# Optimization experiments

Measured on AMD Instinct MI355X. Metric: run time of the kernel, lower is better.

Reference implementation:

```python
import jax, jax.numpy as jnp
import numpy as np

B, S_Q, S_KV, DIM, H = 2, 2048, 2048, 1024, 16
HD = DIM // H
SCALE = HD ** -0.5
EPS = 1e-8


def apply_rope(x, freqs):
    # x: (b, s, h, hd); freqs: (b, s, hd) = [cos | sin] halves of size hd//2
    xr = x.reshape(x.shape[:-1] + (HD // 2, 2))
    x_r, x_i = xr[..., 0], xr[..., 1]
    cos, sin = jnp.split(freqs, 2, axis=-1)          # each (b, s, hd//2)
    cos = cos[:, :, None, :]
    sin = sin[:, :, None, :]
    o_r = x_r * cos - x_i * sin
    o_i = x_r * sin + x_i * cos
    return jnp.stack([o_r, o_i], axis=-1).reshape(x.shape)


def setup_inputs() -> dict:
    key = jax.random.key(0)
    ks = jax.random.split(key, 9)
    q_x = jax.random.normal(ks[0], (B, S_Q, DIM), jnp.float32)
    kv_x = jax.random.normal(ks[1], (B, S_KV, DIM), jnp.float32)
    q_freqs_cis = jax.random.normal(ks[2], (B, S_Q, HD), jnp.float32)
    k_freqs_cis = jax.random.normal(ks[3], (B, S_KV, HD), jnp.float32)
    mask = jnp.zeros((B, 1, S_Q, S_KV), jnp.float32)
    attn_prior = jax.random.uniform(ks[4], (B, S_Q, S_KV), jnp.float32)
    Wq = jax.random.normal(ks[5], (DIM, DIM), jnp.float32) * 0.02
    Wkv = jax.random.normal(ks[6], (2 * DIM, DIM), jnp.float32) * 0.02
    Wproj = jax.random.normal(ks[7], (DIM, DIM), jnp.float32) * 0.02
    bproj = jax.random.normal(ks[8], (DIM,), jnp.float32) * 0.02
    return {"q_x": q_x, "kv_x": kv_x, "q_freqs_cis": q_freqs_cis,
            "k_freqs_cis": k_freqs_cis, "mask": mask, "attn_prior": attn_prior,
            "Wq": Wq, "Wkv": Wkv, "Wproj": Wproj, "bproj": bproj}


def reference(q_x, kv_x, q_freqs_cis, k_freqs_cis, mask, attn_prior,
              Wq, Wkv, Wproj, bproj):
    b, sq, _ = q_x.shape
    skv = kv_x.shape[1]
    q = (q_x @ Wq.T).reshape(b, sq, H, HD)
    kv = (kv_x @ Wkv.T).reshape(b, skv, 2, H, HD)
    k, v = kv[:, :, 0], kv[:, :, 1]
    q = apply_rope(q, q_freqs_cis)
    k = apply_rope(k, k_freqs_cis)
    # scores: (b, h, q, k)
    attn = jnp.einsum("bqhd,bkhd->bhqk", q * SCALE, k)
    attn = attn + mask
    attn = jax.nn.softmax(attn, axis=-1)
    # log-space fusion with multiplicative prior, then renormalize
    prior = attn_prior[:, None, :, :]
    attn = jnp.exp(jnp.log(jnp.clip(attn, EPS)) + jnp.log(jnp.clip(prior, EPS)))
    attn = attn / jnp.sum(attn, axis=-1, keepdims=True)
    x = jnp.einsum("bhqk,bkhd->bqhd", attn, v).reshape(b, sq, DIM)
    x = x @ Wproj.T + bproj
    return (x, attn)
```

## Files before the change

### kernel.cpp

```cpp
#include <hip/hip_runtime.h>
#include <hip/hip_bf16.h>

typedef __bf16 bf16;
typedef __bf16 bf16x4 __attribute__((ext_vector_type(4)));
typedef __bf16 bf16x8 __attribute__((ext_vector_type(8)));
typedef float floatx4 __attribute__((ext_vector_type(4)));
typedef float float4v __attribute__((ext_vector_type(4)));

#define MFMA16(a, b, c) __builtin_amdgcn_mfma_f32_16x16x32_bf16(a, b, c, 0, 0, 0)

constexpr int B_ = 2, S_ = 2048, DIM_ = 1024, H_ = 16, HD_ = 64;
constexpr float SCALE_ = 0.125f;
constexpr float EPS_ = 1e-8f;

__device__ __forceinline__ void gload_lds16(const void* g, void* l) {
    __builtin_amdgcn_global_load_lds(
        (const __attribute__((address_space(1))) void*)g,
        (__attribute__((address_space(3))) void*)l, 16, 0, 0);
}

__global__ __launch_bounds__(256) void prep_kernel(const float* __restrict__ q_x,
                                                   const float* __restrict__ kv_x,
                                                   const float* __restrict__ Wq,
                                                   const float* __restrict__ Wkv,
                                                   const float* __restrict__ Wproj,
                                                   const float* __restrict__ mask,
                                                   const float* __restrict__ prior,
                                                   bf16* __restrict__ qx_b,
                                                   bf16* __restrict__ kvx_b,
                                                   bf16* __restrict__ wq_b,
                                                   bf16* __restrict__ wkv_b,
                                                   bf16* __restrict__ wpj_b,
                                                   float* __restrict__ lp) {
    const int blk = blockIdx.x, t = threadIdx.x;
    auto cvt = [&](const float* in, bf16* out, int base) {
        int i = base * 256 + t;
        float4v v = __builtin_nontemporal_load((const float4v*)in + i);
        bf16x4 o;
#pragma unroll
        for (int j = 0; j < 4; ++j) o[j] = (bf16)v[j];
        ((bf16x4*)out)[i] = o;
    };
    if (blk < 4096)        cvt(q_x,   qx_b,  blk);
    else if (blk < 8192)   cvt(kv_x,  kvx_b, blk - 4096);
    else if (blk < 9216)   cvt(Wq,    wq_b,  blk - 8192);
    else if (blk < 11264)  cvt(Wkv,   wkv_b, blk - 9216);
    else if (blk < 12288)  cvt(Wproj, wpj_b, blk - 11264);
    else {
        int i = (blk - 12288) * 256 + t;
        float4v m = __builtin_nontemporal_load((const float4v*)mask + i);
        float4v p = __builtin_nontemporal_load((const float4v*)prior + i);
        float4v o;
#pragma unroll
        for (int j = 0; j < 4; ++j) o[j] = m[j] + __logf(fmaxf(p[j], EPS_));
        ((float4v*)lp)[i] = o;
    }
}

template<int OUTF32, int BIASED>
__global__ __launch_bounds__(256) void gemm_bt(const bf16* __restrict__ A,
                                               const bf16* __restrict__ B,
                                               void* __restrict__ Cp,
                                               const float* __restrict__ bias,
                                               int M, int N, int K) {
    __shared__ bf16 As[128 * 64];
    __shared__ bf16 Bs[128 * 64];
    const int lane = threadIdx.x & 63, wid = threadIdx.x >> 6;
    const int colL = lane & 15, grp = lane >> 4;
    const int bm = blockIdx.y * 128, bn = blockIdx.x * 128;
    const int wr = wid >> 1, wc = wid & 1;

    floatx4 acc[4][4];
#pragma unroll
    for (int m = 0; m < 4; ++m)
#pragma unroll
        for (int n = 0; n < 4; ++n) acc[m][n] = (floatx4){0.f, 0.f, 0.f, 0.f};

    for (int k0 = 0; k0 < K; k0 += 64) {
#pragma unroll
        for (int i = 0; i < 4; ++i) {
            int c = wid * 256 + i * 64 + lane;
            int row = c >> 3, sub = c & 7;
            gload_lds16(A + (size_t)(bm + row) * K + k0 + sub * 8,
                        &As[(wid * 256 + i * 64) * 8]);
            gload_lds16(B + (size_t)(bn + row) * K + k0 + sub * 8,
                        &Bs[(wid * 256 + i * 64) * 8]);
        }
        __syncthreads();
#pragma unroll
        for (int ks = 0; ks < 2; ++ks) {
            bf16x8 af[4], bfr[4];
#pragma unroll
            for (int m = 0; m < 4; ++m)
                af[m] = *(const bf16x8*)(&As[(wr * 64 + m * 16 + colL) * 64 + ks * 32 + grp * 8]);
#pragma unroll
            for (int n = 0; n < 4; ++n)
                bfr[n] = *(const bf16x8*)(&Bs[(wc * 64 + n * 16 + colL) * 64 + ks * 32 + grp * 8]);
#pragma unroll
            for (int m = 0; m < 4; ++m)
#pragma unroll
                for (int n = 0; n < 4; ++n)
                    acc[m][n] = MFMA16(af[m], bfr[n], acc[m][n]);
        }
        __syncthreads();
    }

#pragma unroll
    for (int m = 0; m < 4; ++m)
#pragma unroll
        for (int n = 0; n < 4; ++n)
#pragma unroll
            for (int r = 0; r < 4; ++r) {
                int row = bm + wr * 64 + m * 16 + grp * 4 + r;
                int col = bn + wc * 64 + n * 16 + colL;
                float v = acc[m][n][r];
                if (BIASED) v += bias[col];
                if (OUTF32)
                    __builtin_nontemporal_store(v, (float*)Cp + (size_t)row * N + col);
                else
                    ((bf16*)Cp)[(size_t)row * N + col] = (bf16)v;
            }
}

__global__ __launch_bounds__(256) void rope_vt_kernel(const bf16* __restrict__ qp,
                                                      const bf16* __restrict__ kvp,
                                                      const float* __restrict__ q_fr,
                                                      const float* __restrict__ k_fr,
                                                      bf16* __restrict__ qr,
                                                      bf16* __restrict__ kr,
                                                      bf16* __restrict__ vt) {
    __shared__ bf16 tile[64][66];
    const int blk = blockIdx.x;
    if (blk < 4096) {
        const bf16* in   = (blk < 2048) ? qp : kvp;
        const float* fr  = (blk < 2048) ? q_fr : k_fr;
        bf16* out        = (blk < 2048) ? qr : kr;
        const int in_ld  = (blk < 2048) ? 1024 : 2048;
        const float scale = (blk < 2048) ? SCALE_ : 1.0f;
        int tid = (blk & 2047) * 256 + threadIdx.x;
        int j = tid & 7, h = (tid >> 3) & 15, s = (tid >> 7) & 2047, b = tid >> 18;
        bf16x8 x = *(const bf16x8*)(in + (size_t)(b * 2048 + s) * in_ld + h * 64 + j * 8);
        const float* f = fr + (size_t)(b * 2048 + s) * 64 + j * 4;
        bf16x8 o;
#pragma unroll
        for (int i = 0; i < 4; ++i) {
            float c = f[i], sn = f[32 + i];
            float x0 = (float)x[2 * i], x1 = (float)x[2 * i + 1];
            o[2 * i]     = (bf16)((x0 * c - x1 * sn) * scale);
            o[2 * i + 1] = (bf16)((x0 * sn + x1 * c) * scale);
        }
        *(bf16x8*)(out + ((size_t)(b * 16 + h) * 2048 + s) * 64 + j * 8) = o;
    } else {
        const int bid = blk - 4096;
        const int sb = bid & 31, h = (bid >> 5) & 15, b = bid >> 9;
        const int tid = threadIdx.x;
#pragma unroll
        for (int i = 0; i < 2; ++i) {
            int c = tid + i * 256;
            int row = c >> 3, sub = c & 7;
            bf16x8 x = *(const bf16x8*)(kvp + (size_t)(b * 2048 + sb * 64 + row) * 2048
                                        + 1024 + h * 64 + sub * 8);
#pragma unroll
            for (int k = 0; k < 8; ++k) tile[row][sub * 8 + k] = x[k];
        }
        __syncthreads();
#pragma unroll
        for (int i = 0; i < 2; ++i) {
            int c = tid + i * 256;
            int drow = c >> 3, sub = c & 7;
            bf16x8 o;
#pragma unroll
            for (int k = 0; k < 8; ++k) o[k] = tile[sub * 8 + k][drow];
            *(bf16x8*)(vt + ((size_t)(b * 16 + h) * 64 + drow) * 2048 + sb * 64 + sub * 8) = o;
        }
    }
}

__global__ __launch_bounds__(256) void attn_fused(const bf16* __restrict__ Qr,
                                                  const bf16* __restrict__ Kr,
                                                  const bf16* __restrict__ Vt,
                                                  const float* __restrict__ lp,
                                                  float* __restrict__ attn_out,
                                                  bf16* __restrict__ O) {
    __shared__ bf16 KB[2][4096];
    __shared__ float LP[2][4096];
    union ShU {
        struct { bf16 VB[2][4096]; bf16 P[4][1024]; } p1;
        float FS[4][1088];
    };
    __shared__ ShU Ush;

    const int tid = threadIdx.x;
    const int lane = tid & 63, wv = tid >> 6;
    const int colL = lane & 15, grp = lane >> 4;
    const int n = blockIdx.x;
    const int x = n & 7, j = n >> 3;
    const int h = j & 15;
    const int pp = (j >> 4) * 8 + x;
    const int b = pp >> 5, qb = pp & 31;
    const int bh = b * H_ + h;
    const int q0 = qb * 64 + wv * 16;
    const int rowL = wv * 16 + colL;

    const bf16* Qbase = Qr + ((size_t)bh * S_ + q0) * HD_;
    const bf16* Kbase = Kr + (size_t)bh * S_ * HD_;
    const bf16* Vbase = Vt + (size_t)bh * HD_ * S_;
    const float* LPbase = lp + ((size_t)b * S_ + qb * 64) * S_;

    bf16x8 qf0 = *(const bf16x8*)(Qbase + (size_t)colL * HD_ + grp * 8);
    bf16x8 qf1 = *(const bf16x8*)(Qbase + (size_t)colL * HD_ + 32 + grp * 8);

    bf16* P = Ush.p1.P[wv];
    const int swz = (colL & 7) << 3;
    const int c7 = colL & 7;

    auto stageK = [&](int buf, int k0) {
#pragma unroll
        for (int i = 0; i < 2; ++i) {
            int c = i * 256 + tid;
            int row = c >> 3, sub = c & 7;
            gload_lds16(Kbase + (size_t)(k0 + row) * HD_ + ((sub ^ (row & 7)) << 3),
                        &KB[buf][(c & ~63) << 3]);
        }
    };
    auto stageV = [&](int buf, int k0) {
#pragma unroll
        for (int i = 0; i < 2; ++i) {
            int c = i * 256 + tid;
            int row = c >> 3, sub = c & 7;
            gload_lds16(Vbase + (size_t)row * S_ + k0 + ((sub ^ (row & 7)) << 3),
                        &Ush.p1.VB[buf][(c & ~63) << 3]);
        }
    };
    auto stageLP = [&](int buf, int k0) {
#pragma unroll
        for (int i = 0; i < 4; ++i) {
            int c = i * 256 + tid;
            int row = c >> 4, col16 = c & 15;
            gload_lds16(LPbase + (size_t)row * S_ + k0 + ((col16 ^ (row & 7)) << 2),
                        &LP[buf][(c & ~63) << 2]);
        }
    };
    auto lpAddr = [&](int ct) {
        return rowL * 64 + (((ct * 4 + grp) ^ (rowL & 7)) << 2);
    };

    float ua = 0.f;
    floatx4 oT[4];
#pragma unroll
    for (int dt = 0; dt < 4; ++dt) oT[dt] = (floatx4){0.f, 0.f, 0.f, 0.f};

    stageK(0, 0);
    stageV(0, 0);
    stageLP(0, 0);
    __syncthreads();

    for (int kt = 0; kt < 32; ++kt) {
        const int k0 = kt * 64;
        const int cur = kt & 1;
        if (kt < 31) {
            stageK(cur ^ 1, k0 + 64);
            stageV(cur ^ 1, k0 + 64);
            stageLP(cur ^ 1, k0 + 64);
        }

        floatx4 s[4];
        __builtin_amdgcn_s_setprio(1);
#pragma unroll
        for (int ct = 0; ct < 4; ++ct) {
            const int r8 = (ct * 16 + colL) * 8;
            bf16x8 a0 = *(const bf16x8*)&KB[cur][(r8 + (grp ^ c7)) * 8];
            bf16x8 a1 = *(const bf16x8*)&KB[cur][(r8 + (grp ^ 4 ^ c7)) * 8];
            floatx4 acc = (floatx4){0.f, 0.f, 0.f, 0.f};
            acc = MFMA16(a0, qf0, acc);
            acc = MFMA16(a1, qf1, acc);
            s[ct] = acc;
        }
        __builtin_amdgcn_s_setprio(0);
#pragma unroll
        for (int ct = 0; ct < 4; ++ct) {
            float4v lv = *(const float4v*)&LP[cur][lpAddr(ct)];
            bf16x4 pw;
#pragma unroll
            for (int r = 0; r < 4; ++r) {
                float tv = __expf(s[ct][r] + lv[r]);
                ua += tv;
                pw[r] = (bf16)tv;
            }
            *(bf16x4*)&P[(colL * 64 + ct * 16 + grp * 4) ^ swz] = pw;
        }
        __builtin_amdgcn_s_setprio(1);
#pragma unroll
        for (int ks = 0; ks < 2; ++ks) {
            bf16x8 pb = *(const bf16x8*)&P[(colL * 64 + ks * 32 + grp * 8) ^ swz];
#pragma unroll
            for (int dt = 0; dt < 4; ++dt) {
                const int r8 = (dt * 16 + colL) * 8;
                bf16x8 vf = *(const bf16x8*)&Ush.p1.VB[cur][(r8 + ((ks * 4 + grp) ^ c7)) * 8];
                oT[dt] = MFMA16(vf, pb, oT[dt]);
            }
        }
        __builtin_amdgcn_s_setprio(0);
        __syncthreads();
    }

    ua += __shfl_xor(ua, 16, 64);
    ua += __shfl_xor(ua, 32, 64);
    const float iu = 1.0f / ua;
#pragma unroll
    for (int dt = 0; dt < 4; ++dt) {
        bf16x4 ow;
#pragma unroll
        for (int r = 0; r < 4; ++r) ow[r] = (bf16)(oT[dt][r] * iu);
        *(bf16x4*)(O + ((size_t)b * S_ + q0 + colL) * DIM_ + h * HD_ + dt * 16 + grp * 4) = ow;
    }

    __syncthreads();
    stageK(0, 0);
    stageLP(0, 0);
    __syncthreads();

    const float* Aout = attn_out + (size_t)bh * S_ * S_;
    for (int kt = 0; kt < 32; ++kt) {
        const int k0 = kt * 64;
        const int cur = kt & 1;
        if (kt < 31) {
            stageK(cur ^ 1, k0 + 64);
            stageLP(cur ^ 1, k0 + 64);
        }

        floatx4 s[4];
        __builtin_amdgcn_s_setprio(1);
#pragma unroll
        for (int ct = 0; ct < 4; ++ct) {
            const int r8 = (ct * 16 + colL) * 8;
            bf16x8 a0 = *(const bf16x8*)&KB[cur][(r8 + (grp ^ c7)) * 8];
            bf16x8 a1 = *(const bf16x8*)&KB[cur][(r8 + (grp ^ 4 ^ c7)) * 8];
            floatx4 acc = (floatx4){0.f, 0.f, 0.f, 0.f};
            acc = MFMA16(a0, qf0, acc);
            acc = MFMA16(a1, qf1, acc);
            s[ct] = acc;
        }
        __builtin_amdgcn_s_setprio(0);
#pragma unroll
        for (int ct = 0; ct < 4; ++ct) {
            float4v lv = *(const float4v*)&LP[cur][lpAddr(ct)];
            float4v o;
#pragma unroll
            for (int r = 0; r < 4; ++r)
                o[r] = __expf(s[ct][r] + lv[r]) * iu;
            *(float4v*)&Ush.FS[wv][colL * 68 + ct * 16 + grp * 4] = o;
        }
#pragma unroll
        for (int it = 0; it < 4; ++it) {
            const int row = it * 4 + grp;
            float4v v = *(const float4v*)&Ush.FS[wv][row * 68 + colL * 4];
            __builtin_nontemporal_store(v,
                (float4v*)(Aout + (size_t)(q0 + row) * S_ + k0 + colL * 4));
        }
        __syncthreads();
    }
}

extern "C" void kernel_launch(void* const* d_in, const int* in_sizes, int n_in,
                              void* d_out, int out_size, void* d_ws, size_t ws_size,
                              hipStream_t stream) {
    const float* q_x   = (const float*)d_in[0];
    const float* kv_x  = (const float*)d_in[1];
    const float* q_fr  = (const float*)d_in[2];
    const float* k_fr  = (const float*)d_in[3];
    const float* maskp = (const float*)d_in[4];
    const float* prior = (const float*)d_in[5];
    const float* Wq    = (const float*)d_in[6];
    const float* Wkv   = (const float*)d_in[7];
    const float* Wproj = (const float*)d_in[8];
    const float* bproj = (const float*)d_in[9];

    float* out_x    = (float*)d_out;
    float* out_attn = out_x + (size_t)B_ * S_ * DIM_;

    char* w = (char*)d_ws;
    bf16* qx_b  = (bf16*)(w + (size_t)0);
    bf16* kvx_b = (bf16*)(w + ((size_t)8  << 20));
    bf16* wq_b  = (bf16*)(w + ((size_t)16 << 20));
    bf16* wkv_b = (bf16*)(w + ((size_t)18 << 20));
    bf16* wpj_b = (bf16*)(w + ((size_t)22 << 20));
    bf16* qp    = (bf16*)(w + ((size_t)24 << 20));
    bf16* kvp   = (bf16*)(w + ((size_t)32 << 20));
    bf16* qr    = (bf16*)(w + ((size_t)48 << 20));
    bf16* kr    = (bf16*)(w + ((size_t)56 << 20));
    bf16* vt    = (bf16*)(w + ((size_t)64 << 20));
    bf16* ob    = (bf16*)(w + ((size_t)72 << 20));
    float* lpb  = (float*)(w + ((size_t)96 << 20));

    prep_kernel<<<20480, 256, 0, stream>>>(q_x, kv_x, Wq, Wkv, Wproj, maskp, prior,
                                           qx_b, kvx_b, wq_b, wkv_b, wpj_b, lpb);

    gemm_bt<0, 0><<<dim3(8, 32),  256, 0, stream>>>(qx_b,  wq_b,  qp,  nullptr, 4096, 1024, 1024);
    gemm_bt<0, 0><<<dim3(16, 32), 256, 0, stream>>>(kvx_b, wkv_b, kvp, nullptr, 4096, 2048, 1024);

    rope_vt_kernel<<<5120, 256, 0, stream>>>(qp, kvp, q_fr, k_fr, qr, kr, vt);

    attn_fused<<<1024, 256, 0, stream>>>(qr, kr, vt, lpb, out_attn, ob);

    gemm_bt<1, 1><<<dim3(8, 32), 256, 0, stream>>>(ob, wpj_b, out_x, bproj, 4096, 1024, 1024);
}
```

Before: 368.3 us.

## Use 128x64 GEMM tiles with XCD-aware block swizzle and 2x-unrolled prep

Result: faster. 358.3 us (-2.7%).

```diff
diff --git a/kernel.cpp b/kernel.cpp
--- a/kernel.cpp
+++ b/kernel.cpp
@@ -34,45 +34,54 @@
                                                    float* __restrict__ lp) {
     const int blk = blockIdx.x, t = threadIdx.x;
     auto cvt = [&](const float* in, bf16* out, int base) {
-        int i = base * 256 + t;
-        float4v v = __builtin_nontemporal_load((const float4v*)in + i);
-        bf16x4 o;
-#pragma unroll
-        for (int j = 0; j < 4; ++j) o[j] = (bf16)v[j];
-        ((bf16x4*)out)[i] = o;
-    };
-    if (blk < 4096)        cvt(q_x,   qx_b,  blk);
-    else if (blk < 8192)   cvt(kv_x,  kvx_b, blk - 4096);
-    else if (blk < 9216)   cvt(Wq,    wq_b,  blk - 8192);
-    else if (blk < 11264)  cvt(Wkv,   wkv_b, blk - 9216);
-    else if (blk < 12288)  cvt(Wproj, wpj_b, blk - 11264);
+#pragma unroll
+        for (int u = 0; u < 2; ++u) {
+            int i = base * 512 + u * 256 + t;
+            float4v v = __builtin_nontemporal_load((const float4v*)in + i);
+            bf16x4 o;
+#pragma unroll
+            for (int j = 0; j < 4; ++j) o[j] = (bf16)v[j];
+            ((bf16x4*)out)[i] = o;
+        }
+    };
+    if (blk < 2048)       cvt(q_x,   qx_b,  blk);
+    else if (blk < 4096)  cvt(kv_x,  kvx_b, blk - 2048);
+    else if (blk < 4608)  cvt(Wq,    wq_b,  blk - 4096);
+    else if (blk < 5632)  cvt(Wkv,   wkv_b, blk - 4608);
+    else if (blk < 6144)  cvt(Wproj, wpj_b, blk - 5632);
     else {
-        int i = (blk - 12288) * 256 + t;
-        float4v m = __builtin_nontemporal_load((const float4v*)mask + i);
-        float4v p = __builtin_nontemporal_load((const float4v*)prior + i);
-        float4v o;
-#pragma unroll
-        for (int j = 0; j < 4; ++j) o[j] = m[j] + __logf(fmaxf(p[j], EPS_));
-        ((float4v*)lp)[i] = o;
+#pragma unroll
+        for (int u = 0; u < 2; ++u) {
+            int i = (blk - 6144) * 512 + u * 256 + t;
+            float4v m = __builtin_nontemporal_load((const float4v*)mask + i);
+            float4v p = __builtin_nontemporal_load((const float4v*)prior + i);
+            float4v o;
+#pragma unroll
+            for (int j = 0; j < 4; ++j) o[j] = m[j] + __logf(fmaxf(p[j], EPS_));
+            ((float4v*)lp)[i] = o;
+        }
     }
 }
 
 template<int OUTF32, int BIASED>
-__global__ __launch_bounds__(256) void gemm_bt(const bf16* __restrict__ A,
-                                               const bf16* __restrict__ B,
-                                               void* __restrict__ Cp,
-                                               const float* __restrict__ bias,
-                                               int M, int N, int K) {
+__global__ __launch_bounds__(256) void gemm_bt64(const bf16* __restrict__ A,
+                                                 const bf16* __restrict__ B,
+                                                 void* __restrict__ Cp,
+                                                 const float* __restrict__ bias,
+                                                 int M, int N, int K) {
     __shared__ bf16 As[128 * 64];
-    __shared__ bf16 Bs[128 * 64];
-    const int lane = threadIdx.x & 63, wid = threadIdx.x >> 6;
+    __shared__ bf16 Bs[64 * 64];
+    const int tid = threadIdx.x;
+    const int lane = tid & 63, wid = tid >> 6;
     const int colL = lane & 15, grp = lane >> 4;
-    const int bm = blockIdx.y * 128, bn = blockIdx.x * 128;
-    const int wr = wid >> 1, wc = wid & 1;
-
-    floatx4 acc[4][4];
-#pragma unroll
-    for (int m = 0; m < 4; ++m)
+    const int nwg = gridDim.x, cpx = nwg >> 3;
+    const int wg = (blockIdx.x & 7) * cpx + (blockIdx.x >> 3);
+    const int nbn = N >> 6;
+    const int bm = (wg / nbn) * 128, bn = (wg % nbn) * 64;
+
+    floatx4 acc[2][4];
+#pragma unroll
+    for (int m = 0; m < 2; ++m)
 #pragma unroll
         for (int n = 0; n < 4; ++n) acc[m][n] = (floatx4){0.f, 0.f, 0.f, 0.f};
 
@@ -82,22 +91,27 @@
             int c = wid * 256 + i * 64 + lane;
             int row = c >> 3, sub = c & 7;
             gload_lds16(A + (size_t)(bm + row) * K + k0 + sub * 8,
-                        &As[(wid * 256 + i * 64) * 8]);
+                        &As[(c & ~63) << 3]);
+        }
+#pragma unroll
+        for (int i = 0; i < 2; ++i) {
+            int c = i * 256 + tid;
+            int row = c >> 3, sub = c & 7;
             gload_lds16(B + (size_t)(bn + row) * K + k0 + sub * 8,
-                        &Bs[(wid * 256 + i * 64) * 8]);
+                        &Bs[(c & ~63) << 3]);
         }
         __syncthreads();
 #pragma unroll
         for (int ks = 0; ks < 2; ++ks) {
-            bf16x8 af[4], bfr[4];
-#pragma unroll
-            for (int m = 0; m < 4; ++m)
-                af[m] = *(const bf16x8*)(&As[(wr * 64 + m * 16 + colL) * 64 + ks * 32 + grp * 8]);
+            bf16x8 af[2], bfr[4];
+#pragma unroll
+            for (int m = 0; m < 2; ++m)
+                af[m] = *(const bf16x8*)(&As[(wid * 32 + m * 16 + colL) * 64 + ks * 32 + grp * 8]);
 #pragma unroll
             for (int n = 0; n < 4; ++n)
-                bfr[n] = *(const bf16x8*)(&Bs[(wc * 64 + n * 16 + colL) * 64 + ks * 32 + grp * 8]);
-#pragma unroll
-            for (int m = 0; m < 4; ++m)
+                bfr[n] = *(const bf16x8*)(&Bs[(n * 16 + colL) * 64 + ks * 32 + grp * 8]);
+#pragma unroll
+            for (int m = 0; m < 2; ++m)
 #pragma unroll
                 for (int n = 0; n < 4; ++n)
                     acc[m][n] = MFMA16(af[m], bfr[n], acc[m][n]);
@@ -106,13 +120,13 @@
     }
 
 #pragma unroll
-    for (int m = 0; m < 4; ++m)
+    for (int m = 0; m < 2; ++m)
 #pragma unroll
         for (int n = 0; n < 4; ++n)
 #pragma unroll
             for (int r = 0; r < 4; ++r) {
-                int row = bm + wr * 64 + m * 16 + grp * 4 + r;
-                int col = bn + wc * 64 + n * 16 + colL;
+                int row = bm + wid * 32 + m * 16 + grp * 4 + r;
+                int col = bn + n * 16 + colL;
                 float v = acc[m][n][r];
                 if (BIASED) v += bias[col];
                 if (OUTF32)
@@ -393,15 +407,15 @@
     bf16* ob    = (bf16*)(w + ((size_t)72 << 20));
     float* lpb  = (float*)(w + ((size_t)96 << 20));
 
-    prep_kernel<<<20480, 256, 0, stream>>>(q_x, kv_x, Wq, Wkv, Wproj, maskp, prior,
+    prep_kernel<<<10240, 256, 0, stream>>>(q_x, kv_x, Wq, Wkv, Wproj, maskp, prior,
                                            qx_b, kvx_b, wq_b, wkv_b, wpj_b, lpb);
 
-    gemm_bt<0, 0><<<dim3(8, 32),  256, 0, stream>>>(qx_b,  wq_b,  qp,  nullptr, 4096, 1024, 1024);
-    gemm_bt<0, 0><<<dim3(16, 32), 256, 0, stream>>>(kvx_b, wkv_b, kvp, nullptr, 4096, 2048, 1024);
+    gemm_bt64<0, 0><<<512,  256, 0, stream>>>(qx_b,  wq_b,  qp,  nullptr, 4096, 1024, 1024);
+    gemm_bt64<0, 0><<<1024, 256, 0, stream>>>(kvx_b, wkv_b, kvp, nullptr, 4096, 2048, 1024);
 
     rope_vt_kernel<<<5120, 256, 0, stream>>>(qp, kvp, q_fr, k_fr, qr, kr, vt);
 
     attn_fused<<<1024, 256, 0, stream>>>(qr, kr, vt, lpb, out_attn, ob);
 
-    gemm_bt<1, 1><<<dim3(8, 32), 256, 0, stream>>>(ob, wpj_b, out_x, bproj, 4096, 1024, 1024);
-}
+    gemm_bt64<1, 1><<<512, 256, 0, stream>>>(ob, wpj_b, out_x, bproj, 4096, 1024, 1024);
+}
```
